# Kernel tuning notes

Hardware: AMD Instinct MI355X
Metric: run time of the kernel (lower is better)

## Reference

```python
import jax, jax.numpy as jnp
import numpy as np

B, NPG, F, DEG = 512, 512, 255, 32   # graphs, nodes-per-graph, feat dim, avg degree
N = B * NPG
E = N * DEG
RATIO = 0.5
K = int(np.ceil(RATIO * NPG))        # nodes kept per graph (static)


def setup_inputs() -> dict:
    key = jax.random.key(0)
    k1, k2, k3, k4, k5 = jax.random.split(key, 5)
    out = jax.random.normal(k1, (N, F), jnp.float32)
    z = jax.random.randint(k2, (N,), 0, 101)  # z == 100 marks virtual nodes
    # random edges strictly within each graph (block-contiguous node ids)
    local = jax.random.randint(k3, (2, B, NPG * DEG), 0, NPG)
    offs = (jnp.arange(B) * NPG)[None, :, None]
    edge_index = (local + offs).reshape(2, E)
    batch = jnp.repeat(jnp.arange(B), NPG)
    W = jax.random.normal(k4, (F + 1, 1), jnp.float32) * (1.0 / np.sqrt(F + 1))
    b = jnp.zeros((1,), jnp.float32)
    edge_attr = jax.random.normal(k5, (E, 1), jnp.float32)  # carried but unused by SAGPool scoring
    return dict(out=out, z=z, edge_index=edge_index, batch=batch, W=W, b=b,
                edge_attr=edge_attr)


def gcn_score(x, edge_index, W, b):
    """GCNConv(F+1 -> 1) with self-loops and symmetric normalization."""
    n = x.shape[0]
    h = (x @ W)[:, 0]  # [N] since out_channels == 1
    row, col = edge_index[0], edge_index[1]
    loop = jnp.arange(n)
    row = jnp.concatenate([row, loop])
    col = jnp.concatenate([col, loop])
    deg = jax.ops.segment_sum(jnp.ones_like(col, x.dtype), col, num_segments=n)
    dinv = jnp.where(deg > 0, jax.lax.rsqrt(deg), 0.0)
    norm = dinv[row] * dinv[col]  # deg^-1/2 * deg^-1/2 per edge
    agg = jax.ops.segment_sum(norm * h[row], col, num_segments=n)
    return agg + b[0]


def reference(out, z, edge_index, batch, W, b, edge_attr):
    # concat real/virtual bit
    real = (z != 100).astype(out.dtype)[:, None]
    x = jnp.concatenate([out, real], axis=-1)          # [N, F+1]
    # SAGPooling: score nodes, tanh nonlinearity
    score = jnp.tanh(gcn_score(x, edge_index, W, b))   # [N]
    # per-graph top-k (uniform graph size -> static-shape top_k)
    sv, si = jax.lax.top_k(score.reshape(B, NPG), K)   # [B, K]
    perm = (si + (jnp.arange(B) * NPG)[:, None]).reshape(-1)  # global node ids
    xp = x[perm] * sv.reshape(-1)[:, None]             # gated selected nodes [B*K, F+1]
    # global_mean_pool over pooled batch (k nodes per graph)
    return xp.reshape(B, K, F + 1).mean(axis=1)        # [B, F+1]
```

## Files before the change

### kernel.cpp

```cpp
#include <hip/hip_runtime.h>
#include <math.h>

#define NPG     512
#define B_GR    512
#define FDIM    255
#define DEG     32
#define EPG     (NPG * DEG)
#define N_NODES (B_GR * NPG)
#define E_TOT   (N_NODES * DEG)
#define K_KEEP  256
#define GRP_TOT (N_NODES / 4)

__global__ __launch_bounds__(256) void k_proj(const float* __restrict__ feat,
                                              const int*   __restrict__ z,
                                              const float* __restrict__ W,
                                              float*       __restrict__ h) {
    __shared__ __align__(16) float Wx[1020];
    __shared__ float w255s;

    const int tid = threadIdx.x;
    for (int k = tid; k < 1020; k += 256) Wx[k] = W[k % 255];
    if (tid == 0) w255s = W[255];
    __syncthreads();

    const int lane = tid & 63;
    const int wv   = tid >> 6;
    const float4* W4 = (const float4*)Wx;
    const float4* F4 = (const float4*)feat;
    const int4*   Z4 = (const int4*)z;
    float4*       H4 = (float4*)h;
    const float w255 = w255s;
    const bool  l63  = (lane == 63);

    const float4 wf0 = W4[lane];
    const float4 wf1 = W4[64 + lane];
    const float4 wf2 = W4[128 + lane];
    const float4 wf3 = l63 ? make_float4(0.f, 0.f, 0.f, 0.f) : W4[192 + lane];

    const int nwaves = gridDim.x * 4;
    for (int grp = blockIdx.x * 4 + wv; grp < GRP_TOT; grp += nwaves) {
        const float4* src = F4 + (size_t)grp * 255;
        const float4 a = src[lane];
        const float4 b = src[64 + lane];
        const float4 c = src[128 + lane];
        const float4 d = l63 ? make_float4(0.f, 0.f, 0.f, 0.f) : src[192 + lane];

        float acc0 = a.x * wf0.x + a.y * wf0.y + a.z * wf0.z;
        const float p03 = a.w * wf0.w;
        float acc1 = b.x * wf1.x + b.y * wf1.y;
        const float p12 = b.z * wf1.z, p13 = b.w * wf1.w;
        float acc2 = c.x * wf2.x;
        const float p21 = c.y * wf2.y, p22 = c.z * wf2.z, p23 = c.w * wf2.w;
        float acc3 = d.x * wf3.x + d.y * wf3.y + d.z * wf3.z + d.w * wf3.w;

        const float q03 = p03;
        const float q1  = p12 + p13;
        const float q2  = p21 + p22 + p23;
        acc0 += l63 ? 0.f : q03;
        acc1 += l63 ? q03 : q1;
        acc2 += l63 ? q1  : q2;
        acc3 += l63 ? q2  : 0.f;

#pragma unroll
        for (int off = 32; off; off >>= 1) {
            acc0 += __shfl_down(acc0, off, 64);
            acc1 += __shfl_down(acc1, off, 64);
            acc2 += __shfl_down(acc2, off, 64);
            acc3 += __shfl_down(acc3, off, 64);
        }
        if (lane == 0) {
            const int4 zz = Z4[grp];
            float4 hv;
            hv.x = acc0 + ((zz.x != 100) ? w255 : 0.f);
            hv.y = acc1 + ((zz.y != 100) ? w255 : 0.f);
            hv.z = acc2 + ((zz.z != 100) ? w255 : 0.f);
            hv.w = acc3 + ((zz.w != 100) ? w255 : 0.f);
            H4[grp] = hv;
        }
    }
}

__global__ __launch_bounds__(1024) void k_score(const float* __restrict__ feat,
                                                const int*   __restrict__ z,
                                                const int*   __restrict__ ei,
                                                const float* __restrict__ bias,
                                                const float* __restrict__ h,
                                                float*       __restrict__ outp) {
    __shared__ ushort4 cc4[EPG / 4];
    __shared__ __align__(16) float score[NPG];
    __shared__ float v_l[NPG];
    __shared__ float dinv_l[NPG];
    __shared__ float agg[NPG];
    __shared__ float realb[NPG];
    __shared__ int   deg[NPG];
    __shared__ int   rank2[2][NPG];
    __shared__ int   selidx[K_KEEP];
    __shared__ float selsc[K_KEEP];
    __shared__ float red[3][256];
    __shared__ int   cnt;

    const int g     = blockIdx.x;
    const int tid   = threadIdx.x;
    const int nbase = g * NPG;

    const int4* colp4 = (const int4*)(ei + (size_t)E_TOT + (size_t)g * EPG);
    const int4* rowp4 = (const int4*)(ei + (size_t)g * EPG);

    if (tid < NPG) {
        v_l[tid]   = h[nbase + tid];
        realb[tid] = (z[nbase + tid] != 100) ? 1.f : 0.f;
        deg[tid]   = 1;
    }
    if (tid == 0) cnt = 0;
    __syncthreads();

#pragma unroll
    for (int it = 0; it < 4; ++it) {
        const int  idx = it * 1024 + tid;
        const int4 c4  = colp4[idx];
        ushort4 u;
        u.x = (unsigned short)(c4.x - nbase);
        u.y = (unsigned short)(c4.y - nbase);
        u.z = (unsigned short)(c4.z - nbase);
        u.w = (unsigned short)(c4.w - nbase);
        cc4[idx] = u;
        atomicAdd(&deg[u.x], 1);
        atomicAdd(&deg[u.y], 1);
        atomicAdd(&deg[u.z], 1);
        atomicAdd(&deg[u.w], 1);
    }
    __syncthreads();

    if (tid < NPG) {
        const float di = (float)(1.0 / sqrt((double)deg[tid]));
        dinv_l[tid] = di;
        const float v = di * v_l[tid];
        v_l[tid] = v;
        agg[tid] = v;
    }
    __syncthreads();

#pragma unroll
    for (int it = 0; it < 4; ++it) {
        const int     idx = it * 1024 + tid;
        const int4    r4  = rowp4[idx];
        const ushort4 u   = cc4[idx];
        atomicAdd(&agg[u.x], v_l[r4.x - nbase]);
        atomicAdd(&agg[u.y], v_l[r4.y - nbase]);
        atomicAdd(&agg[u.z], v_l[r4.z - nbase]);
        atomicAdd(&agg[u.w], v_l[r4.w - nbase]);
    }
    __syncthreads();

    if (tid < NPG)
        score[tid] = tanhf(fmaf(agg[tid], dinv_l[tid], bias[0]));
    __syncthreads();

    {
        const int     node = tid & (NPG - 1);
        const int     half = tid >> 9;
        const float   sc   = score[node];
        const float4* s4p  = (const float4*)&score[half * 256];
        int part = 0;
#pragma unroll 8
        for (int i = 0; i < 64; ++i) {
            const float4 s4 = s4p[i];
            const int    j  = half * 256 + i * 4;
            part += (s4.x > sc) || (s4.x == sc && (j + 0) < node);
            part += (s4.y > sc) || (s4.y == sc && (j + 1) < node);
            part += (s4.z > sc) || (s4.z == sc && (j + 2) < node);
            part += (s4.w > sc) || (s4.w == sc && (j + 3) < node);
        }
        rank2[half][node] = part;
    }
    __syncthreads();

    if (tid < NPG) {
        const int rank = rank2[0][tid] + rank2[1][tid];
        if (rank < K_KEEP) {
            const int slot = atomicAdd(&cnt, 1);
            selidx[slot] = tid;
            selsc[slot]  = score[tid];
        }
    }
    __syncthreads();

    {
        const int f = tid & 255;
        const int q = tid >> 8;
        float acc = 0.f;
        if (f < FDIM) {
            const float* fb = feat + (size_t)nbase * FDIM + f;
#pragma unroll
            for (int k = 0; k < 64; k += 8) {
                int   is[8]; float ss[8]; float tv[8];
#pragma unroll
                for (int j = 0; j < 8; ++j) {
                    is[j] = selidx[q + 4 * (k + j)];
                    ss[j] = selsc [q + 4 * (k + j)];
                }
#pragma unroll
                for (int j = 0; j < 8; ++j)
                    tv[j] = fb[(size_t)is[j] * FDIM];
#pragma unroll
                for (int j = 0; j < 8; ++j)
                    acc = fmaf(ss[j], tv[j], acc);
            }
        } else {
            for (int s = q; s < K_KEEP; s += 4)
                acc = fmaf(selsc[s], realb[selidx[s]], acc);
        }
        if (q) red[q - 1][f] = acc;
        __syncthreads();
        if (q == 0)
            outp[(size_t)g * 256 + f] =
                (acc + red[0][f] + red[1][f] + red[2][f]) * (1.f / K_KEEP);
    }
}

extern "C" void kernel_launch(void* const* d_in, const int* in_sizes, int n_in,
                              void* d_out, int out_size, void* d_ws, size_t ws_size,
                              hipStream_t stream) {
    const float* feat = (const float*)d_in[0];
    const int*   z    = (const int*)  d_in[1];
    const int*   ei   = (const int*)  d_in[2];
    const float* W    = (const float*)d_in[4];
    const float* bias = (const float*)d_in[5];
    float* outp = (float*)d_out;
    float* h    = (float*)d_ws;

    k_proj <<<2048, 256,  0, stream>>>(feat, z, W, h);
    k_score<<<B_GR, 1024, 0, stream>>>(feat, z, ei, bias, h, outp);
}
```

Baseline: 125.3 us.

## Fuse projection kernel into per-graph scoring kernel

Folds the node-feature projection (x·W) into the per-graph scoring kernel, so each block computes h for its own 512 nodes directly into shared memory instead of round-tripping through a workspace buffer and a second launch. It also hoists all row and column edge loads into registers up front so they overlap with the degree atomics. The aim is to cut a launch and the h global write/read and to warm the cache with this graph's features before the gather. The cost is a longer serial phase per block and higher register pressure, and the launch bounds now request eight blocks of minimum occupancy.

```diff
diff --git a/kernel.cpp b/kernel.cpp
--- a/kernel.cpp
+++ b/kernel.cpp
@@ -9,86 +9,17 @@
 #define N_NODES (B_GR * NPG)
 #define E_TOT   (N_NODES * DEG)
 #define K_KEEP  256
-#define GRP_TOT (N_NODES / 4)
-
-__global__ __launch_bounds__(256) void k_proj(const float* __restrict__ feat,
-                                              const int*   __restrict__ z,
-                                              const float* __restrict__ W,
-                                              float*       __restrict__ h) {
+
+__global__ __launch_bounds__(1024, 8) void k_fused(const float* __restrict__ feat,
+                                                   const int*   __restrict__ z,
+                                                   const int*   __restrict__ ei,
+                                                   const float* __restrict__ W,
+                                                   const float* __restrict__ bias,
+                                                   float*       __restrict__ outp) {
+    __shared__ ushort4 cc4[EPG / 4];
     __shared__ __align__(16) float Wx[1020];
-    __shared__ float w255s;
-
-    const int tid = threadIdx.x;
-    for (int k = tid; k < 1020; k += 256) Wx[k] = W[k % 255];
-    if (tid == 0) w255s = W[255];
-    __syncthreads();
-
-    const int lane = tid & 63;
-    const int wv   = tid >> 6;
-    const float4* W4 = (const float4*)Wx;
-    const float4* F4 = (const float4*)feat;
-    const int4*   Z4 = (const int4*)z;
-    float4*       H4 = (float4*)h;
-    const float w255 = w255s;
-    const bool  l63  = (lane == 63);
-
-    const float4 wf0 = W4[lane];
-    const float4 wf1 = W4[64 + lane];
-    const float4 wf2 = W4[128 + lane];
-    const float4 wf3 = l63 ? make_float4(0.f, 0.f, 0.f, 0.f) : W4[192 + lane];
-
-    const int nwaves = gridDim.x * 4;
-    for (int grp = blockIdx.x * 4 + wv; grp < GRP_TOT; grp += nwaves) {
-        const float4* src = F4 + (size_t)grp * 255;
-        const float4 a = src[lane];
-        const float4 b = src[64 + lane];
-        const float4 c = src[128 + lane];
-        const float4 d = l63 ? make_float4(0.f, 0.f, 0.f, 0.f) : src[192 + lane];
-
-        float acc0 = a.x * wf0.x + a.y * wf0.y + a.z * wf0.z;
-        const float p03 = a.w * wf0.w;
-        float acc1 = b.x * wf1.x + b.y * wf1.y;
-        const float p12 = b.z * wf1.z, p13 = b.w * wf1.w;
-        float acc2 = c.x * wf2.x;
-        const float p21 = c.y * wf2.y, p22 = c.z * wf2.z, p23 = c.w * wf2.w;
-        float acc3 = d.x * wf3.x + d.y * wf3.y + d.z * wf3.z + d.w * wf3.w;
-
-        const float q03 = p03;
-        const float q1  = p12 + p13;
-        const float q2  = p21 + p22 + p23;
-        acc0 += l63 ? 0.f : q03;
-        acc1 += l63 ? q03 : q1;
-        acc2 += l63 ? q1  : q2;
-        acc3 += l63 ? q2  : 0.f;
-
-#pragma unroll
-        for (int off = 32; off; off >>= 1) {
-            acc0 += __shfl_down(acc0, off, 64);
-            acc1 += __shfl_down(acc1, off, 64);
-            acc2 += __shfl_down(acc2, off, 64);
-            acc3 += __shfl_down(acc3, off, 64);
-        }
-        if (lane == 0) {
-            const int4 zz = Z4[grp];
-            float4 hv;
-            hv.x = acc0 + ((zz.x != 100) ? w255 : 0.f);
-            hv.y = acc1 + ((zz.y != 100) ? w255 : 0.f);
-            hv.z = acc2 + ((zz.z != 100) ? w255 : 0.f);
-            hv.w = acc3 + ((zz.w != 100) ? w255 : 0.f);
-            H4[grp] = hv;
-        }
-    }
-}
-
-__global__ __launch_bounds__(1024) void k_score(const float* __restrict__ feat,
-                                                const int*   __restrict__ z,
-                                                const int*   __restrict__ ei,
-                                                const float* __restrict__ bias,
-                                                const float* __restrict__ h,
-                                                float*       __restrict__ outp) {
-    __shared__ ushort4 cc4[EPG / 4];
     __shared__ __align__(16) float score[NPG];
-    __shared__ float v_l[NPG];
+    __shared__ __align__(16) float v_l[NPG];
     __shared__ float dinv_l[NPG];
     __shared__ float agg[NPG];
     __shared__ float realb[NPG];
@@ -97,60 +28,125 @@
     __shared__ int   selidx[K_KEEP];
     __shared__ float selsc[K_KEEP];
     __shared__ float red[3][256];
+    __shared__ float w255s;
     __shared__ int   cnt;
 
     const int g     = blockIdx.x;
     const int tid   = threadIdx.x;
     const int nbase = g * NPG;
+    const int lane  = tid & 63;
+    const int wave  = tid >> 6;
 
     const int4* colp4 = (const int4*)(ei + (size_t)E_TOT + (size_t)g * EPG);
     const int4* rowp4 = (const int4*)(ei + (size_t)g * EPG);
 
+    if (tid < 1020) Wx[tid] = W[tid % 255];
+    if (tid == 0) { w255s = W[255]; cnt = 0; }
     if (tid < NPG) {
-        v_l[tid]   = h[nbase + tid];
         realb[tid] = (z[nbase + tid] != 100) ? 1.f : 0.f;
         deg[tid]   = 1;
     }
-    if (tid == 0) cnt = 0;
-    __syncthreads();
-
-#pragma unroll
-    for (int it = 0; it < 4; ++it) {
-        const int  idx = it * 1024 + tid;
-        const int4 c4  = colp4[idx];
-        ushort4 u;
-        u.x = (unsigned short)(c4.x - nbase);
-        u.y = (unsigned short)(c4.y - nbase);
-        u.z = (unsigned short)(c4.z - nbase);
-        u.w = (unsigned short)(c4.w - nbase);
-        cc4[idx] = u;
-        atomicAdd(&deg[u.x], 1);
-        atomicAdd(&deg[u.y], 1);
-        atomicAdd(&deg[u.z], 1);
-        atomicAdd(&deg[u.w], 1);
-    }
-    __syncthreads();
-
-    if (tid < NPG) {
-        const float di = (float)(1.0 / sqrt((double)deg[tid]));
-        dinv_l[tid] = di;
-        const float v = di * v_l[tid];
-        v_l[tid] = v;
-        agg[tid] = v;
-    }
-    __syncthreads();
-
-#pragma unroll
-    for (int it = 0; it < 4; ++it) {
-        const int     idx = it * 1024 + tid;
-        const int4    r4  = rowp4[idx];
-        const ushort4 u   = cc4[idx];
-        atomicAdd(&agg[u.x], v_l[r4.x - nbase]);
-        atomicAdd(&agg[u.y], v_l[r4.y - nbase]);
-        atomicAdd(&agg[u.z], v_l[r4.z - nbase]);
-        atomicAdd(&agg[u.w], v_l[r4.w - nbase]);
-    }
-    __syncthreads();
+    __syncthreads();
+
+    {
+        const bool l63 = (lane == 63);
+        const float4 zero = make_float4(0.f, 0.f, 0.f, 0.f);
+        const float4* W4 = (const float4*)Wx;
+        const float4 wf0 = W4[lane];
+        const float4 wf1 = W4[64 + lane];
+        const float4 wf2 = W4[128 + lane];
+        const float4 wf3 = l63 ? zero : W4[192 + lane];
+        const float  w255 = w255s;
+        const float4* F4 = (const float4*)(feat + (size_t)nbase * FDIM);
+        float4* v4 = (float4*)v_l;
+
+        for (int k = 0; k < 8; ++k) {
+            const int grp = wave + (k << 4);
+            const float4* src = F4 + (size_t)grp * 255;
+            const float4 a = src[lane];
+            const float4 b = src[64 + lane];
+            const float4 c = src[128 + lane];
+            const float4 d = l63 ? zero : src[192 + lane];
+
+            float acc0 = a.x * wf0.x + a.y * wf0.y + a.z * wf0.z;
+            const float p03 = a.w * wf0.w;
+            float acc1 = b.x * wf1.x + b.y * wf1.y;
+            const float p12 = b.z * wf1.z, p13 = b.w * wf1.w;
+            float acc2 = c.x * wf2.x;
+            const float p21 = c.y * wf2.y, p22 = c.z * wf2.z, p23 = c.w * wf2.w;
+            float acc3 = d.x * wf3.x + d.y * wf3.y + d.z * wf3.z + d.w * wf3.w;
+
+            const float q03 = p03;
+            const float q1  = p12 + p13;
+            const float q2  = p21 + p22 + p23;
+            acc0 += l63 ? 0.f : q03;
+            acc1 += l63 ? q03 : q1;
+            acc2 += l63 ? q1  : q2;
+            acc3 += l63 ? q2  : 0.f;
+
+#pragma unroll
+            for (int off = 32; off; off >>= 1) {
+                acc0 += __shfl_down(acc0, off, 64);
+                acc1 += __shfl_down(acc1, off, 64);
+                acc2 += __shfl_down(acc2, off, 64);
+                acc3 += __shfl_down(acc3, off, 64);
+            }
+            if (lane == 0) {
+                const int n0 = grp * 4;
+                float4 hv;
+                hv.x = acc0 + realb[n0 + 0] * w255;
+                hv.y = acc1 + realb[n0 + 1] * w255;
+                hv.z = acc2 + realb[n0 + 2] * w255;
+                hv.w = acc3 + realb[n0 + 3] * w255;
+                v4[grp] = hv;
+            }
+        }
+    }
+    __syncthreads();
+
+    {
+        int4 c4v[4], r4v[4];
+#pragma unroll
+        for (int it = 0; it < 4; ++it) c4v[it] = colp4[it * 1024 + tid];
+#pragma unroll
+        for (int it = 0; it < 4; ++it) r4v[it] = rowp4[it * 1024 + tid];
+
+#pragma unroll
+        for (int it = 0; it < 4; ++it) {
+            const int4 c4 = c4v[it];
+            ushort4 u;
+            u.x = (unsigned short)(c4.x - nbase);
+            u.y = (unsigned short)(c4.y - nbase);
+            u.z = (unsigned short)(c4.z - nbase);
+            u.w = (unsigned short)(c4.w - nbase);
+            cc4[it * 1024 + tid] = u;
+            atomicAdd(&deg[u.x], 1);
+            atomicAdd(&deg[u.y], 1);
+            atomicAdd(&deg[u.z], 1);
+            atomicAdd(&deg[u.w], 1);
+        }
+        __syncthreads();
+
+        if (tid < NPG) {
+            const float di = (float)(1.0 / sqrt((double)deg[tid]));
+            dinv_l[tid] = di;
+            const float v = di * v_l[tid];
+            v_l[tid] = v;
+            agg[tid] = v;
+        }
+        __syncthreads();
+
+#pragma unroll
+        for (int it = 0; it < 4; ++it) {
+            const ushort4 u  = cc4[it * 1024 + tid];
+            const int4    r4 = r4v[it];
+            atomicAdd(&agg[u.x], v_l[r4.x - nbase]);
+            atomicAdd(&agg[u.y], v_l[r4.y - nbase]);
+            atomicAdd(&agg[u.z], v_l[r4.z - nbase]);
+            atomicAdd(&agg[u.w], v_l[r4.w - nbase]);
+        }
+        __syncthreads();
+    }
 
     if (tid < NPG)
         score[tid] = tanhf(fmaf(agg[tid], dinv_l[tid], bias[0]));
@@ -227,8 +223,6 @@
     const float* W    = (const float*)d_in[4];
     const float* bias = (const float*)d_in[5];
     float* outp = (float*)d_out;
-    float* h    = (float*)d_ws;
-
-    k_proj <<<2048, 256,  0, stream>>>(feat, z, W, h);
-    k_score<<<B_GR, 1024, 0, stream>>>(feat, z, ei, bias, h, outp);
+
+    k_fused<<<B_GR, 1024, 0, stream>>>(feat, z, ei, W, bias, outp);
 }
```

After: 131.1 us. +4.6%, slower.
